# Optimization experiments

Hardware: AMD Instinct MI355X
Metric: run time of the kernel (lower is better)

The kernel has to match this reference:

```python
import jax, jax.numpy as jnp
import numpy as np

H = 2048        # hidden_size
NH = 16         # num query heads
NKV = 4         # num kv heads
HD = H // NH    # head_dim = 128
G = NH // NKV   # kv groups = 4
EPS = 1e-12


def setup_inputs() -> dict:
    key = jax.random.key(0)
    ks = jax.random.split(key, 20)
    B, S = 2, 2048
    s = 1.0 / np.sqrt(H)
    inp = {
        "hidden_states": jax.random.normal(ks[0], (B, S, H), jnp.float32),
        "source_states": jax.random.normal(ks[1], (B, S, H), jnp.float32),
        # weights stored [in, out] so y = x @ W + b
        "Wq": jax.random.normal(ks[2], (H, NH * HD), jnp.float32) * s,
        "bq": jnp.zeros((NH * HD,), jnp.float32),
        "Wk": jax.random.normal(ks[3], (H, NKV * HD), jnp.float32) * s,
        "bk": jnp.zeros((NKV * HD,), jnp.float32),
        "Wv": jax.random.normal(ks[4], (H, NKV * HD), jnp.float32) * s,
        "bv": jnp.zeros((NKV * HD,), jnp.float32),
        "Wd": jax.random.normal(ks[5], (H, H), jnp.float32) * s,
        "bd": jnp.zeros((H,), jnp.float32),
        "W1": jax.random.normal(ks[6], (H, H), jnp.float32) * s,
        "b1": jnp.zeros((H,), jnp.float32),
        "W2": jax.random.normal(ks[7], (H, H), jnp.float32) * s,
        "b2": jnp.zeros((H,), jnp.float32),
        "gamma": jnp.ones((H,), jnp.float32),
        "beta": jnp.zeros((H,), jnp.float32),
    }
    return inp


def _layernorm(x, gamma, beta):
    mu = jnp.mean(x, axis=-1, keepdims=True)
    var = jnp.mean(jnp.square(x - mu), axis=-1, keepdims=True)
    return (x - mu) * jax.lax.rsqrt(var + EPS) * gamma + beta


def reference(hidden_states, source_states, Wq, bq, Wk, bk, Wv, bv, Wd, bd,
              W1, b1, W2, b2, gamma, beta):
    B, Sq, _ = hidden_states.shape
    Ss = source_states.shape[1]
    # FFN-gate on source: Pl1 = relu(lin1(src)); P = lin2(Pl1) + Pl1
    Pl1 = jax.nn.relu(source_states @ W1 + b1)
    P = (Pl1 @ W2 + b2) + Pl1
    # projections; K/V grouped into NKV heads, Q into NH = NKV*G heads
    K = (P @ Wk + bk).reshape(B, Ss, NKV, HD).transpose(0, 2, 1, 3)        # b k s d
    V = (P @ Wv + bv).reshape(B, Ss, NKV, HD).transpose(0, 2, 1, 3)        # b k s d
    Q = (hidden_states @ Wq + bq).reshape(B, Sq, NKV, G, HD)
    Q = Q.transpose(0, 2, 3, 1, 4)                                          # b k g q d
    scores = jnp.einsum('bkgqd,bksd->bkgqs', Q, K) / np.sqrt(HD)
    probs = jax.nn.softmax(scores, axis=-1)
    ctx = jnp.einsum('bkgqs,bksd->bkgqd', probs, V)                         # b k g q d
    ctx = ctx.transpose(0, 3, 1, 2, 4).reshape(B, Sq, NH * HD)              # b q h*d
    out = ctx @ Wd + bd
    return _layernorm(out + hidden_states, gamma, beta)
```

## Files before the change

kernel.cpp:

```cpp
#include <hip/hip_runtime.h>
#include <hip/hip_bf16.h>

typedef __bf16 bf16;
typedef __bf16 bf16x4 __attribute__((ext_vector_type(4)));
typedef __bf16 bf16x8 __attribute__((ext_vector_type(8)));
typedef float  f32x4  __attribute__((ext_vector_type(4)));

#define H_   2048
#define S_   2048
#define B_   2
#define NH_  16
#define NKV_ 4
#define HD_  128
#define KVS  1024

__device__ __forceinline__ f32x4 mfma16(bf16x8 a, bf16x8 b, f32x4 c) {
  return __builtin_amdgcn_mfma_f32_16x16x32_bf16(a, b, c, 0, 0, 0);
}

typedef __attribute__((address_space(3))) unsigned int lds_u32_t;
typedef const __attribute__((address_space(1))) unsigned int glb_u32_t;
__device__ __forceinline__ void glds16(const bf16* g, bf16* l) {
  __builtin_amdgcn_global_load_lds((glb_u32_t*)g, (lds_u32_t*)l, 16, 0, 0);
}

__global__ __launch_bounds__(256)
void f2b(const float* __restrict__ in, bf16* __restrict__ out)
{
  const size_t i = ((size_t)blockIdx.x * 256 + threadIdx.x) * 4;
  const float4 v = *(const float4*)(in + i);
  bf16x4 o = { (bf16)v.x, (bf16)v.y, (bf16)v.z, (bf16)v.w };
  *(bf16x4*)(out + i) = o;
}

__global__ __launch_bounds__(256)
void transpose_f2b(const float* __restrict__ in, bf16* __restrict__ out, int K, int N)
{
  __shared__ bf16 t[32][33];
  const int tx = threadIdx.x & 31, ty = threadIdx.x >> 5;
  const int k0 = blockIdx.x * 32, n0 = blockIdx.y * 32;
  #pragma unroll
  for (int i = 0; i < 4; i++)
    t[ty + i*8][tx] = (bf16)in[(size_t)(k0 + ty + i*8) * N + n0 + tx];
  __syncthreads();
  #pragma unroll
  for (int i = 0; i < 4; i++)
    out[(size_t)(n0 + ty + i*8) * K + k0 + tx] = t[tx][ty + i*8];
}

__global__ __launch_bounds__(256)
void concat_bias(const float* __restrict__ bk, const float* __restrict__ bv,
                 float* __restrict__ bkv)
{
  const int i = blockIdx.x * 256 + threadIdx.x;
  bkv[i] = (i < 512) ? bk[i] : bv[i - 512];
}

__global__ __launch_bounds__(256)
void transpose_v(const bf16* __restrict__ KVin, bf16* __restrict__ Vt)
{
  __shared__ bf16 t[32][33];
  const int tx = threadIdx.x & 31, ty = threadIdx.x >> 5;
  const int s0 = blockIdx.x * 32, d0 = blockIdx.y * 32;
  const int bk = blockIdx.z;
  const int b = bk >> 2, kv = bk & 3;
  const bf16* src = KVin + (size_t)b * S_ * KVS + 512 + kv * HD_;
  #pragma unroll
  for (int i = 0; i < 4; i++)
    t[ty + i*8][tx] = src[(size_t)(s0 + ty + i*8) * KVS + d0 + tx];
  __syncthreads();
  bf16* dst = Vt + (size_t)bk * HD_ * S_;
  #pragma unroll
  for (int i = 0; i < 4; i++)
    dst[(size_t)(d0 + ty + i*8) * S_ + s0 + tx] = t[tx][ty + i*8];
}

__global__ __launch_bounds__(256)
void gemm128(const bf16* __restrict__ A, const bf16* __restrict__ Wt,
             const float* __restrict__ bias, const bf16* __restrict__ resid,
             bf16* __restrict__ outB, int N, int K, int relu)
{
  __shared__ __align__(16) bf16 As[128][32];
  __shared__ __align__(16) bf16 Bs[128][32];
  const int tid  = threadIdx.x;
  const int lane = tid & 63;
  const int w    = tid >> 6;
  const int wm = w & 1, wn = w >> 1;
  const int quad = lane >> 4, l16 = lane & 15;
  const int m0 = blockIdx.y * 128;
  const int n0 = blockIdx.x * 128;

  const int g_r = lane >> 2;
  const int g_c = (lane & 3) * 8;
  bf16* AsF = &As[0][0];
  bf16* BsF = &Bs[0][0];

  const f32x4 fz = {0.f, 0.f, 0.f, 0.f};
  f32x4 acc[4][4];
  #pragma unroll
  for (int i = 0; i < 4; i++)
    #pragma unroll
    for (int j = 0; j < 4; j++) acc[i][j] = fz;

  for (int k0 = 0; k0 < K; k0 += 32) {
    __syncthreads();
    #pragma unroll
    for (int i = 0; i < 2; i++) {
      const int rb = (w*2 + i) * 16;
      glds16(A  + (size_t)(m0 + rb + g_r) * K + k0 + g_c, AsF + rb*32 + lane*8);
      glds16(Wt + (size_t)(n0 + rb + g_r) * K + k0 + g_c, BsF + rb*32 + lane*8);
    }
    __syncthreads();
    bf16x8 af[4], bfr[4];
    #pragma unroll
    for (int i = 0; i < 4; i++) af[i]  = *(const bf16x8*)(&As[wm*64 + i*16 + l16][quad*8]);
    #pragma unroll
    for (int j = 0; j < 4; j++) bfr[j] = *(const bf16x8*)(&Bs[wn*64 + j*16 + l16][quad*8]);
    #pragma unroll
    for (int i = 0; i < 4; i++)
      #pragma unroll
      for (int j = 0; j < 4; j++)
        acc[i][j] = mfma16(af[i], bfr[j], acc[i][j]);
  }

  #pragma unroll
  for (int i = 0; i < 4; i++) {
    const int row = m0 + wm*64 + i*16 + quad*4;
    #pragma unroll
    for (int j = 0; j < 4; j++) {
      const int col = n0 + wn*64 + j*16 + l16;
      const float bi = bias[col];
      #pragma unroll
      for (int r = 0; r < 4; r++) {
        float v = acc[i][j][r] + bi;
        if (relu) v = fmaxf(v, 0.f);
        size_t idx = (size_t)(row + r) * N + col;
        if (resid) v += (float)resid[idx];
        outB[idx] = (bf16)v;
      }
    }
  }
}

__global__ __launch_bounds__(256)
void attn_partial(const bf16* __restrict__ Q, const bf16* __restrict__ KV,
                  const bf16* __restrict__ Vt, bf16* __restrict__ OpBase,
                  float* __restrict__ LsBase)
{
  __shared__ __align__(16) bf16 Ks[2][4][32][32];
  __shared__ __align__(16) bf16 Vs[2][8][16][32];
  __shared__ __align__(16) bf16 Ps[4][32][40];
  const int tid = threadIdx.x;
  const int lane = tid & 63, w = tid >> 6;
  const int quad = lane >> 4, l16 = lane & 15;
  const int qt = blockIdx.x, h = blockIdx.y;
  const int b = blockIdx.z >> 1, sh = blockIdx.z & 1;
  const int kv = h >> 2;
  const int qbase = qt * 128 + w * 32;
  const int s_begin = sh * (S_/2);

  bf16*  Op = OpBase + (size_t)sh * 8388608;
  float* Lp = LsBase + (size_t)sh * (B_*NH_*S_);

  const bf16* Qp = Q  + ((size_t)b * S_ + qbase) * H_ + h * HD_;
  const bf16* Kp = KV + (size_t)b * S_ * KVS + kv * HD_;
  const bf16* Vp = Vt + (size_t)(b * NKV_ + kv) * HD_ * S_;

  const int g_r = lane >> 2;
  const int g_c = (lane & 3) * 8;

  const f32x4 fz = {0.f, 0.f, 0.f, 0.f};

  bf16x8 qf[2][4];
  #pragma unroll
  for (int i = 0; i < 2; i++)
    #pragma unroll
    for (int kt = 0; kt < 4; kt++)
      qf[i][kt] = *(const bf16x8*)(Qp + (size_t)(i*16 + l16) * H_ + kt*32 + quad*8);

  f32x4 o[2][8];
  #pragma unroll
  for (int i = 0; i < 2; i++)
    #pragma unroll
    for (int n = 0; n < 8; n++) o[i][n] = fz;
  float lsum[2][4];
  #pragma unroll
  for (int i = 0; i < 2; i++)
    #pragma unroll
    for (int r = 0; r < 4; r++) lsum[i][r] = 0.f;

  const float scale = 0.08838834764831845f;
  const int rd_sw = ((l16 >> 2) & 3) * 8;

  {
    const int s0 = s_begin;
    glds16(Kp + (size_t)(s0 +      g_r) * KVS + w*32 + g_c, &Ks[0][w][0][0]   + lane*8);
    glds16(Kp + (size_t)(s0 + 16 + g_r) * KVS + w*32 + g_c, &Ks[0][w][16][0]  + lane*8);
    glds16(Vp + (size_t)(w*16     + g_r) * S_ + s0 + g_c,   &Vs[0][w][0][0]   + lane*8);
    glds16(Vp + (size_t)((4+w)*16 + g_r) * S_ + s0 + g_c,   &Vs[0][4+w][0][0] + lane*8);
  }

  const int NIT = (S_/2) / 32;
  for (int it = 0; it < NIT; it++) {
    const int bf = it & 1;
    __syncthreads();
    if (it + 1 < NIT) {
      const int s0 = s_begin + (it + 1) * 32;
      const int nb = bf ^ 1;
      glds16(Kp + (size_t)(s0 +      g_r) * KVS + w*32 + g_c, &Ks[nb][w][0][0]   + lane*8);
      glds16(Kp + (size_t)(s0 + 16 + g_r) * KVS + w*32 + g_c, &Ks[nb][w][16][0]  + lane*8);
      glds16(Vp + (size_t)(w*16     + g_r) * S_ + s0 + g_c,   &Vs[nb][w][0][0]   + lane*8);
      glds16(Vp + (size_t)((4+w)*16 + g_r) * S_ + s0 + g_c,   &Vs[nb][4+w][0][0] + lane*8);
    }

    f32x4 sa[2][2];
    sa[0][0] = fz; sa[0][1] = fz; sa[1][0] = fz; sa[1][1] = fz;
    #pragma unroll
    for (int kt = 0; kt < 4; kt++) {
      bf16x8 kf0 = *(const bf16x8*)(&Ks[bf][kt][l16][quad*8]);
      bf16x8 kf1 = *(const bf16x8*)(&Ks[bf][kt][16 + l16][quad*8]);
      #pragma unroll
      for (int i = 0; i < 2; i++) {
        sa[i][0] = mfma16(qf[i][kt], kf0, sa[i][0]);
        sa[i][1] = mfma16(qf[i][kt], kf1, sa[i][1]);
      }
    }
    #pragma unroll
    for (int i = 0; i < 2; i++)
      #pragma unroll
      for (int nt = 0; nt < 2; nt++)
        #pragma unroll
        for (int r = 0; r < 4; r++) {
          float p = __expf(sa[i][nt][r] * scale);
          lsum[i][r] += p;
          Ps[w][i*16 + quad*4 + r][(nt*16 + l16) ^ (quad*8)] = (bf16)p;
        }
    bf16x8 pf[2];
    #pragma unroll
    for (int i = 0; i < 2; i++)
      pf[i] = *(const bf16x8*)(&Ps[w][i*16 + l16][(quad*8) ^ rd_sw]);
    #pragma unroll
    for (int nt = 0; nt < 8; nt++) {
      bf16x8 vf = *(const bf16x8*)(&Vs[bf][nt][l16][quad*8]);
      #pragma unroll
      for (int i = 0; i < 2; i++)
        o[i][nt] = mfma16(pf[i], vf, o[i][nt]);
    }
  }

  #pragma unroll
  for (int i = 0; i < 2; i++)
    #pragma unroll
    for (int r = 0; r < 4; r++) {
      float s = lsum[i][r];
      s += __shfl_xor(s, 1);
      s += __shfl_xor(s, 2);
      s += __shfl_xor(s, 4);
      s += __shfl_xor(s, 8);
      lsum[i][r] = s;
    }

  bf16* op = Op + ((size_t)b * S_ + qbase) * H_ + h * HD_;
  #pragma unroll
  for (int i = 0; i < 2; i++)
    #pragma unroll
    for (int nt = 0; nt < 8; nt++)
      #pragma unroll
      for (int r = 0; r < 4; r++)
        op[(size_t)(i*16 + quad*4 + r) * H_ + nt*16 + l16] = (bf16)o[i][nt][r];
  if (l16 == 0) {
    float* lp = Lp + (size_t)(b * NH_ + h) * S_ + qbase;
    #pragma unroll
    for (int i = 0; i < 2; i++)
      #pragma unroll
      for (int r = 0; r < 4; r++)
        lp[i*16 + quad*4 + r] = lsum[i][r];
  }
}

__global__ __launch_bounds__(256)
void attn_combine(const bf16* __restrict__ O0, const bf16* __restrict__ O1,
                  const float* __restrict__ L0, const float* __restrict__ L1,
                  bf16* __restrict__ ctx)
{
  const int row = blockIdx.x;
  const int b = row >> 11, s = row & 2047;
  const int tid = threadIdx.x;
  const int h = tid >> 4;
  const size_t idx = (size_t)row * H_ + tid * 8;
  const size_t li  = (size_t)(b * NH_ + h) * S_ + s;
  const float rinv = 1.f / (L0[li] + L1[li]);
  bf16x8 a = *(const bf16x8*)(O0 + idx);
  bf16x8 c = *(const bf16x8*)(O1 + idx);
  bf16x8 o;
  #pragma unroll
  for (int k = 0; k < 8; k++)
    o[k] = (bf16)(((float)a[k] + (float)c[k]) * rinv);
  *(bf16x8*)(ctx + idx) = o;
}

__global__ __launch_bounds__(256)
void ln_fused(const bf16* __restrict__ a, const float* __restrict__ hidden,
              const float* __restrict__ gamma, const float* __restrict__ beta,
              float* __restrict__ out)
{
  __shared__ float red[8];
  const int row = blockIdx.x;
  const bf16*  pa = a      + (size_t)row * H_;
  const float* pb = hidden + (size_t)row * H_;
  float x[8]; float s = 0.f, s2 = 0.f;
  #pragma unroll
  for (int j = 0; j < 8; j++) {
    int c = threadIdx.x + j*256;
    float v = (float)pa[c] + pb[c];
    x[j] = v; s += v; s2 += v*v;
  }
  #pragma unroll
  for (int off = 1; off < 64; off <<= 1) {
    s  += __shfl_xor(s,  off);
    s2 += __shfl_xor(s2, off);
  }
  const int wv = threadIdx.x >> 6;
  if ((threadIdx.x & 63) == 0) { red[wv] = s; red[4 + wv] = s2; }
  __syncthreads();
  s  = red[0] + red[1] + red[2] + red[3];
  s2 = red[4] + red[5] + red[6] + red[7];
  const float mu   = s * (1.0f / H_);
  const float var  = s2 * (1.0f / H_) - mu * mu;
  const float rstd = rsqrtf(var + 1e-12f);
  float* po = out + (size_t)row * H_;
  #pragma unroll
  for (int j = 0; j < 8; j++) {
    int c = threadIdx.x + j*256;
    po[c] = ((x[j] - mu) * rstd) * gamma[c] + beta[c];
  }
}

extern "C" void kernel_launch(void* const* d_in, const int* in_sizes, int n_in,
                              void* d_out, int out_size, void* d_ws, size_t ws_size,
                              hipStream_t stream)
{
  (void)in_sizes; (void)n_in; (void)out_size; (void)ws_size;
  const float* hidden = (const float*)d_in[0];
  const float* source = (const float*)d_in[1];
  const float* Wq = (const float*)d_in[2];
  const float* bq = (const float*)d_in[3];
  const float* Wk = (const float*)d_in[4];
  const float* bk = (const float*)d_in[5];
  const float* Wv = (const float*)d_in[6];
  const float* bv = (const float*)d_in[7];
  const float* Wd = (const float*)d_in[8];
  const float* bd = (const float*)d_in[9];
  const float* W1 = (const float*)d_in[10];
  const float* b1 = (const float*)d_in[11];
  const float* W2 = (const float*)d_in[12];
  const float* b2 = (const float*)d_in[13];
  const float* gamma = (const float*)d_in[14];
  const float* beta  = (const float*)d_in[15];

  char* ws = (char*)d_ws;
  const size_t M = 1048576;
  bf16*  rA   = (bf16*)(ws + 0*M);
  bf16*  rB   = (bf16*)(ws + 16*M);
  bf16*  Qb   = (bf16*)(ws + 32*M);
  bf16*  Wt_  = (bf16*)(ws + 48*M);
  bf16*  rE   = (bf16*)(ws + 56*M);
  bf16*  Wkvt = (bf16*)(ws + 72*M);
  bf16*  KVb  = (bf16*)(ws + 76*M);
  bf16*  Vtb  = (bf16*)(ws + 84*M);
  float* Ls   = (float*)(ws + 48*M);
  float* bkv  = (float*)(ws + 48*M + 524288);
  bf16*  O0 = rA;
  bf16*  O1 = rB;

  f2b<<<8192, 256, 0, stream>>>(hidden, rA );
  transpose_f2b<<<dim3(64,64), 256, 0, stream>>>(Wq, Wt_, 2048, 2048);
  gemm128<<<dim3(16,32), 256, 0, stream>>>(rA, Wt_, bq, nullptr, Qb, 2048, 2048, 0);

  f2b<<<8192, 256, 0, stream>>>(source, rB );
  transpose_f2b<<<dim3(64,64), 256, 0, stream>>>(W1, Wt_, 2048, 2048);
  gemm128<<<dim3(16,32), 256, 0, stream>>>(rB, Wt_, b1, nullptr, rA , 2048, 2048, 1);
  transpose_f2b<<<dim3(64,64), 256, 0, stream>>>(W2, Wt_, 2048, 2048);
  gemm128<<<dim3(16,32), 256, 0, stream>>>(rA, Wt_, b2, rA , rE , 2048, 2048, 0);

  transpose_f2b<<<dim3(64,16), 256, 0, stream>>>(Wk, Wkvt, 2048, 512);
  transpose_f2b<<<dim3(64,16), 256, 0, stream>>>(Wv, Wkvt + (size_t)512*2048, 2048, 512);
  concat_bias<<<4, 256, 0, stream>>>(bk, bv, bkv);
  gemm128<<<dim3(8,32), 256, 0, stream>>>(rE, Wkvt, bkv, nullptr, KVb, 1024, 2048, 0);
  transpose_v<<<dim3(64,4,8), 256, 0, stream>>>(KVb, Vtb);

  attn_partial<<<dim3(16,16,4), 256, 0, stream>>>(Qb, KVb, Vtb, O0, Ls);
  attn_combine<<<4096, 256, 0, stream>>>(O0, O1, Ls, Ls + B_*NH_*S_,
                                         rE );

  transpose_f2b<<<dim3(64,64), 256, 0, stream>>>(Wd, Wt_, 2048, 2048);
  gemm128<<<dim3(16,32), 256, 0, stream>>>(rE, Wt_, bd, nullptr, rA , 2048, 2048, 0);
  ln_fused<<<4096, 256, 0, stream>>>(rA, hidden, gamma, beta, (float*)d_out);
}
```

Measured before the change: 623.6 us.

## Double-buffer GEMM LDS, batch Q and lin1 GEMMs, fold softmax scale into Q

The GEMM now uses two LDS buffers so the next K-slice loads while the current slice runs MFMAs, removing one barrier-bound stall per iteration. The Q projection and the first FFN GEMM run in a single dual launch with twice the blocks, and the two fp32-to-bf16 conversions share one launch. The softmax scale times log2(e) is applied in the Q projection epilogue, so attention can use exp2f without a multiply. The cost is doubled LDS per block, which can lower occupancy, and Q is rounded to bf16 after scaling, which changes rounding slightly.

```diff
diff --git a/kernel.cpp b/kernel.cpp
--- a/kernel.cpp
+++ b/kernel.cpp
@@ -14,6 +14,8 @@
 #define HD_  128
 #define KVS  1024
 
+#define QSCALE 0.12751743f
+
 __device__ __forceinline__ f32x4 mfma16(bf16x8 a, bf16x8 b, f32x4 c) {
   return __builtin_amdgcn_mfma_f32_16x16x32_bf16(a, b, c, 0, 0, 0);
 }
@@ -25,8 +27,11 @@
 }
 
 __global__ __launch_bounds__(256)
-void f2b(const float* __restrict__ in, bf16* __restrict__ out)
-{
+void f2b2(const float* __restrict__ i0, bf16* __restrict__ o0,
+          const float* __restrict__ i1, bf16* __restrict__ o1)
+{
+  const float* in = blockIdx.z ? i1 : i0;
+  bf16*       out = blockIdx.z ? o1 : o0;
   const size_t i = ((size_t)blockIdx.x * 256 + threadIdx.x) * 4;
   const float4 v = *(const float4*)(in + i);
   bf16x4 o = { (bf16)v.x, (bf16)v.y, (bf16)v.z, (bf16)v.w };
@@ -75,25 +80,19 @@
     dst[(size_t)(d0 + ty + i*8) * S_ + s0 + tx] = t[tx][ty + i*8];
 }
 
-__global__ __launch_bounds__(256)
-void gemm128(const bf16* __restrict__ A, const bf16* __restrict__ Wt,
-             const float* __restrict__ bias, const bf16* __restrict__ resid,
-             bf16* __restrict__ outB, int N, int K, int relu)
-{
-  __shared__ __align__(16) bf16 As[128][32];
-  __shared__ __align__(16) bf16 Bs[128][32];
+__device__ __forceinline__
+void gemm_body(const bf16* __restrict__ A, const bf16* __restrict__ Wt,
+               const float* __restrict__ bias, const bf16* __restrict__ resid,
+               bf16* __restrict__ outB, int N, int K, int relu, float oscale,
+               int m0, int n0, bf16* As, bf16* Bs)
+{
   const int tid  = threadIdx.x;
   const int lane = tid & 63;
   const int w    = tid >> 6;
   const int wm = w & 1, wn = w >> 1;
   const int quad = lane >> 4, l16 = lane & 15;
-  const int m0 = blockIdx.y * 128;
-  const int n0 = blockIdx.x * 128;
-
   const int g_r = lane >> 2;
   const int g_c = (lane & 3) * 8;
-  bf16* AsF = &As[0][0];
-  bf16* BsF = &Bs[0][0];
 
   const f32x4 fz = {0.f, 0.f, 0.f, 0.f};
   f32x4 acc[4][4];
@@ -102,20 +101,28 @@
     #pragma unroll
     for (int j = 0; j < 4; j++) acc[i][j] = fz;
 
-  for (int k0 = 0; k0 < K; k0 += 32) {
-    __syncthreads();
+  auto stage = [&](int nb, int k0) {
     #pragma unroll
     for (int i = 0; i < 2; i++) {
       const int rb = (w*2 + i) * 16;
-      glds16(A  + (size_t)(m0 + rb + g_r) * K + k0 + g_c, AsF + rb*32 + lane*8);
-      glds16(Wt + (size_t)(n0 + rb + g_r) * K + k0 + g_c, BsF + rb*32 + lane*8);
-    }
+      glds16(A  + (size_t)(m0 + rb + g_r) * K + k0 + g_c, As + nb*4096 + rb*32 + lane*8);
+      glds16(Wt + (size_t)(n0 + rb + g_r) * K + k0 + g_c, Bs + nb*4096 + rb*32 + lane*8);
+    }
+  };
+
+  stage(0, 0);
+  const int NK = K >> 5;
+  for (int it = 0; it < NK; it++) {
+    const int bf = it & 1;
     __syncthreads();
+    if (it + 1 < NK) stage(bf ^ 1, (it + 1) << 5);
     bf16x8 af[4], bfr[4];
     #pragma unroll
-    for (int i = 0; i < 4; i++) af[i]  = *(const bf16x8*)(&As[wm*64 + i*16 + l16][quad*8]);
-    #pragma unroll
-    for (int j = 0; j < 4; j++) bfr[j] = *(const bf16x8*)(&Bs[wn*64 + j*16 + l16][quad*8]);
+    for (int i = 0; i < 4; i++)
+      af[i]  = *(const bf16x8*)(As + bf*4096 + (wm*64 + i*16 + l16)*32 + quad*8);
+    #pragma unroll
+    for (int j = 0; j < 4; j++)
+      bfr[j] = *(const bf16x8*)(Bs + bf*4096 + (wn*64 + j*16 + l16)*32 + quad*8);
     #pragma unroll
     for (int i = 0; i < 4; i++)
       #pragma unroll
@@ -134,12 +141,42 @@
       for (int r = 0; r < 4; r++) {
         float v = acc[i][j][r] + bi;
         if (relu) v = fmaxf(v, 0.f);
+        v *= oscale;
         size_t idx = (size_t)(row + r) * N + col;
         if (resid) v += (float)resid[idx];
         outB[idx] = (bf16)v;
       }
     }
   }
+}
+
+__global__ __launch_bounds__(256)
+void gemm_one(const bf16* __restrict__ A, const bf16* __restrict__ Wt,
+              const float* __restrict__ bias, const bf16* __restrict__ resid,
+              bf16* __restrict__ outB, int N, int K, int relu, float oscale)
+{
+  __shared__ __align__(16) bf16 As[2*128*32];
+  __shared__ __align__(16) bf16 Bs[2*128*32];
+  gemm_body(A, Wt, bias, resid, outB, N, K, relu, oscale,
+            blockIdx.y*128, blockIdx.x*128, As, Bs);
+}
+
+__global__ __launch_bounds__(256)
+void gemm_dual(const bf16* __restrict__ A0, const bf16* __restrict__ W0,
+               const float* __restrict__ b0, bf16* __restrict__ o0,
+               int relu0, float s0,
+               const bf16* __restrict__ A1, const bf16* __restrict__ W1,
+               const float* __restrict__ b1, bf16* __restrict__ o1,
+               int relu1, float s1, int N, int K)
+{
+  __shared__ __align__(16) bf16 As[2*128*32];
+  __shared__ __align__(16) bf16 Bs[2*128*32];
+  if (blockIdx.z == 0)
+    gemm_body(A0, W0, b0, nullptr, o0, N, K, relu0, s0,
+              blockIdx.y*128, blockIdx.x*128, As, Bs);
+  else
+    gemm_body(A1, W1, b1, nullptr, o1, N, K, relu1, s1,
+              blockIdx.y*128, blockIdx.x*128, As, Bs);
 }
 
 __global__ __launch_bounds__(256)
@@ -189,7 +226,6 @@
     #pragma unroll
     for (int r = 0; r < 4; r++) lsum[i][r] = 0.f;
 
-  const float scale = 0.08838834764831845f;
   const int rd_sw = ((l16 >> 2) & 3) * 8;
 
   {
@@ -231,7 +267,7 @@
       for (int nt = 0; nt < 2; nt++)
         #pragma unroll
         for (int r = 0; r < 4; r++) {
-          float p = __expf(sa[i][nt][r] * scale);
+          float p = exp2f(sa[i][nt][r]);
           lsum[i][r] += p;
           Ps[w][i*16 + quad*4 + r][(nt*16 + l16) ^ (quad*8)] = (bf16)p;
         }
@@ -363,8 +399,10 @@
   bf16*  rA   = (bf16*)(ws + 0*M);
   bf16*  rB   = (bf16*)(ws + 16*M);
   bf16*  Qb   = (bf16*)(ws + 32*M);
-  bf16*  Wt_  = (bf16*)(ws + 48*M);
+  bf16*  WtA  = (bf16*)(ws + 48*M);
   bf16*  rE   = (bf16*)(ws + 56*M);
+  bf16*  rF   = (bf16*)(ws + 72*M);
+  bf16*  Pl1  = rF;
   bf16*  Wkvt = (bf16*)(ws + 72*M);
   bf16*  KVb  = (bf16*)(ws + 76*M);
   bf16*  Vtb  = (bf16*)(ws + 84*M);
@@ -372,28 +410,24 @@
   float* bkv  = (float*)(ws + 48*M + 524288);
   bf16*  O0 = rA;
   bf16*  O1 = rB;
-
-  f2b<<<8192, 256, 0, stream>>>(hidden, rA );
-  transpose_f2b<<<dim3(64,64), 256, 0, stream>>>(Wq, Wt_, 2048, 2048);
-  gemm128<<<dim3(16,32), 256, 0, stream>>>(rA, Wt_, bq, nullptr, Qb, 2048, 2048, 0);
-
-  f2b<<<8192, 256, 0, stream>>>(source, rB );
-  transpose_f2b<<<dim3(64,64), 256, 0, stream>>>(W1, Wt_, 2048, 2048);
-  gemm128<<<dim3(16,32), 256, 0, stream>>>(rB, Wt_, b1, nullptr, rA , 2048, 2048, 1);
-  transpose_f2b<<<dim3(64,64), 256, 0, stream>>>(W2, Wt_, 2048, 2048);
-  gemm128<<<dim3(16,32), 256, 0, stream>>>(rA, Wt_, b2, rA , rE , 2048, 2048, 0);
-
+  bf16*  oFb = Qb;
+
+  transpose_f2b<<<dim3(64,64), 256, 0, stream>>>(Wq, WtA, 2048, 2048);
+  transpose_f2b<<<dim3(64,64), 256, 0, stream>>>(W1, rE,  2048, 2048);
+  f2b2<<<dim3(8192,1,2), 256, 0, stream>>>(hidden, rA, source, rB);
+  gemm_dual<<<dim3(16,32,2), 256, 0, stream>>>(
+      rA, WtA, bq, Qb,  0, QSCALE,
+      rB, rE,  b1, Pl1, 1, 1.0f, 2048, 2048);
+  transpose_f2b<<<dim3(64,64), 256, 0, stream>>>(W2, WtA, 2048, 2048);
+  gemm_one<<<dim3(16,32), 256, 0, stream>>>(Pl1, WtA, b2, Pl1, rE , 2048, 2048, 0, 1.0f);
   transpose_f2b<<<dim3(64,16), 256, 0, stream>>>(Wk, Wkvt, 2048, 512);
   transpose_f2b<<<dim3(64,16), 256, 0, stream>>>(Wv, Wkvt + (size_t)512*2048, 2048, 512);
   concat_bias<<<4, 256, 0, stream>>>(bk, bv, bkv);
-  gemm128<<<dim3(8,32), 256, 0, stream>>>(rE, Wkvt, bkv, nullptr, KVb, 1024, 2048, 0);
+  gemm_one<<<dim3(8,32), 256, 0, stream>>>(rE, Wkvt, bkv, nullptr, KVb, 1024, 2048, 0, 1.0f);
   transpose_v<<<dim3(64,4,8), 256, 0, stream>>>(KVb, Vtb);
-
   attn_partial<<<dim3(16,16,4), 256, 0, stream>>>(Qb, KVb, Vtb, O0, Ls);
-  attn_combine<<<4096, 256, 0, stream>>>(O0, O1, Ls, Ls + B_*NH_*S_,
-                                         rE );
-
-  transpose_f2b<<<dim3(64,64), 256, 0, stream>>>(Wd, Wt_, 2048, 2048);
-  gemm128<<<dim3(16,32), 256, 0, stream>>>(rE, Wt_, bd, nullptr, rA , 2048, 2048, 0);
-  ln_fused<<<4096, 256, 0, stream>>>(rA, hidden, gamma, beta, (float*)d_out);
-}
+  attn_combine<<<4096, 256, 0, stream>>>(O0, O1, Ls, Ls + B_*NH_*S_, rE);
+  transpose_f2b<<<dim3(64,64), 256, 0, stream>>>(Wd, WtA, 2048, 2048);
+  gemm_one<<<dim3(16,32), 256, 0, stream>>>(rE, WtA, bd, nullptr, oFb, 2048, 2048, 0, 1.0f);
+  ln_fused<<<4096, 256, 0, stream>>>(oFb, hidden, gamma, beta, (float*)d_out);
+}
```

Measured after the change: 609.1 us. 2.3% less time.
